# Kernel tuning notes

Measured on AMD Instinct MI355X. Metric: run time of the kernel, lower is better.

Reference implementation:

```python
import jax, jax.numpy as jnp
import numpy as np

B, T, C, H = 2, 2048, 1024, 16
D = C // H  # head dim = 64
NEG_MIN = jnp.finfo(jnp.float32).min


def setup_inputs() -> dict:
    key = jax.random.key(0)
    ks = jax.random.split(key, 5)
    std = 0.02
    return {
        "x": jax.random.normal(ks[0], (B, T, C), dtype=jnp.float32),
        "Wq": std * jax.random.normal(ks[1], (C, C), dtype=jnp.float32),
        "bq": jnp.zeros((C,), dtype=jnp.float32),
        "Wk": std * jax.random.normal(ks[2], (C, C), dtype=jnp.float32),
        "bk": jnp.zeros((C,), dtype=jnp.float32),
        "Wv": std * jax.random.normal(ks[3], (C, C), dtype=jnp.float32),
        "bv": jnp.zeros((C,), dtype=jnp.float32),
        "Wo": (std / np.sqrt(24.0)) * jax.random.normal(ks[4], (C, C), dtype=jnp.float32),
        "bo": jnp.zeros((C,), dtype=jnp.float32),
    }


def reference(x, Wq, bq, Wk, bk, Wv, bv, Wo, bo):
    # QKV projections -> (B, H, T, D)
    def proj(W, b):
        return (x @ W + b).reshape(B, T, H, D).transpose(0, 2, 1, 3)

    q = proj(Wq, bq)
    k = proj(Wk, bk)
    v = proj(Wv, bv)

    # full scores (B, H, T, T), causal mask, softmax
    attn = jnp.einsum("bhqd,bhkd->bhqk", q, k) / jnp.sqrt(jnp.float32(D))
    mask = jnp.tril(jnp.ones((T, T), dtype=bool))[None, None]
    attn = jnp.where(mask, attn, NEG_MIN)
    scores = jax.nn.softmax(attn, axis=-1)

    out = jnp.einsum("bhqk,bhkd->bhqd", scores, v)
    out = out.transpose(0, 2, 1, 3).reshape(B, T, C)
    return out @ Wo + bo
```

## Files before the change

### kernel.cpp

```cpp
#include <hip/hip_runtime.h>
#include <stdint.h>
#include <stddef.h>


#define B_SZ 2
#define T_SZ 2048
#define C_SZ 1024
#define H_SZ 16
#define D_SZ 64
#define M_SZ (B_SZ * T_SZ)
#define BHTD (B_SZ * H_SZ * T_SZ * D_SZ)
#define CC (C_SZ * C_SZ)

typedef __attribute__((ext_vector_type(8))) __bf16 bf16x8;
typedef __attribute__((ext_vector_type(4))) float f32x4;
typedef __attribute__((ext_vector_type(16))) float f32x16;

__device__ __forceinline__ unsigned short f2bf(float f) {
    union { float f; unsigned u; } v; v.f = f;
    v.u += 0x7fffu + ((v.u >> 16) & 1u);
    return (unsigned short)(v.u >> 16);
}

__device__ __forceinline__ unsigned pkbf(float lo, float hi_) {
    union { unsigned u; __bf16 h[2]; } r;
    r.h[0] = (__bf16)lo; r.h[1] = (__bf16)hi_;
    return r.u;
}

__device__ __forceinline__ float fexp2(float x) {
    float r;
    asm volatile("v_exp_f32 %0, %1\n\ts_nop 0" : "=v"(r) : "v"(x));
    return r;
}

__device__ __forceinline__ void load_lds16(const unsigned short* g, unsigned short* l) {
    __builtin_amdgcn_global_load_lds(
        (const __attribute__((address_space(1))) void*)g,
        (__attribute__((address_space(3))) void*)l, 16, 0, 0);
}


__global__ void cvt_x_kernel(const float4* __restrict__ in, ushort4* __restrict__ out, int n4) {
    int stride = gridDim.x * blockDim.x;
    for (int i = blockIdx.x * blockDim.x + threadIdx.x; i < n4; i += stride) {
        float4 v = in[i];
        ushort4 o;
        o.x = f2bf(v.x); o.y = f2bf(v.y); o.z = f2bf(v.z); o.w = f2bf(v.w);
        out[i] = o;
    }
}

__global__ __launch_bounds__(256) void transpose_cvt_kernel(
    const float* __restrict__ W0, const float* __restrict__ W1,
    const float* __restrict__ W2, const float* __restrict__ W3,
    unsigned short* __restrict__ T0, unsigned short* __restrict__ T1,
    unsigned short* __restrict__ T2, unsigned short* __restrict__ T3)
{
    __shared__ float tile[32][33];
    const float* W; unsigned short* Wt;
    switch (blockIdx.z) {
        case 0: W = W0; Wt = T0; break;
        case 1: W = W1; Wt = T1; break;
        case 2: W = W2; Wt = T2; break;
        default: W = W3; Wt = T3; break;
    }
    const int tx = threadIdx.x, ty = threadIdx.y;
    const int n0 = blockIdx.x * 32, k0 = blockIdx.y * 32;
    #pragma unroll
    for (int i = 0; i < 4; i++)
        tile[ty + i * 8][tx] = W[(size_t)(k0 + ty + i * 8) * C_SZ + n0 + tx];
    __syncthreads();
    #pragma unroll
    for (int i = 0; i < 4; i++)
        Wt[(size_t)(n0 + ty + i * 8) * C_SZ + k0 + tx] = f2bf(tile[tx][ty + i * 8]);
}

__global__ __launch_bounds__(256) void vt_kernel(
    const unsigned short* __restrict__ V, unsigned short* __restrict__ Vt)
{
    __shared__ unsigned short tile[32][33];
    const int bh = blockIdx.z;
    const int t0 = blockIdx.x * 32, d0 = blockIdx.y * 32;
    const unsigned short* src = V + (size_t)bh * T_SZ * D_SZ;
    unsigned short* dst = Vt + (size_t)bh * T_SZ * D_SZ;
    const int tx = threadIdx.x, ty = threadIdx.y;
    #pragma unroll
    for (int i = 0; i < 4; i++)
        tile[ty + i * 8][tx] = src[(size_t)(t0 + ty + i * 8) * D_SZ + d0 + tx];
    __syncthreads();
    #pragma unroll
    for (int i = 0; i < 4; i++)
        dst[(size_t)(d0 + ty + i * 8) * T_SZ + t0 + tx] = tile[tx][ty + i * 8];
}


__device__ __forceinline__ void gemm_tile_core(
    const unsigned short* __restrict__ A,
    const unsigned short* __restrict__ Bt,
    unsigned short* As, unsigned short* Bs,
    int m0, int n0, f32x4 acc[4][4])
{
    const int tid = threadIdx.x;
    const int lane = tid & 63;
    const int w = tid >> 6;
    const int l15 = lane & 15, lg = lane >> 4;
    const int wr = (w >> 1) * 64, wc = (w & 1) * 64;

    const unsigned short* Ag0 = A + (size_t)(m0 + (tid >> 2)) * C_SZ + (tid & 3) * 8;
    const unsigned short* Ag1 = Ag0 + (size_t)64 * C_SZ;
    const unsigned short* Bg0 = Bt + (size_t)(n0 + (tid >> 2)) * C_SZ + (tid & 3) * 8;
    const unsigned short* Bg1 = Bg0 + (size_t)64 * C_SZ;
    unsigned short* As0 = As + w * 512;
    unsigned short* As1 = As + 2048 + w * 512;
    unsigned short* Bs0 = Bs + w * 512;
    unsigned short* Bs1 = Bs + 2048 + w * 512;

    for (int k0 = 0; k0 < C_SZ; k0 += 32) {
        load_lds16(Ag0 + k0, As0);
        load_lds16(Ag1 + k0, As1);
        load_lds16(Bg0 + k0, Bs0);
        load_lds16(Bg1 + k0, Bs1);
        __syncthreads();
        bf16x8 af[4], bfv[4];
        const bf16x8* Ap = (const bf16x8*)As;
        const bf16x8* Bp = (const bf16x8*)Bs;
        #pragma unroll
        for (int m = 0; m < 4; m++) af[m] = Ap[(wr + m * 16 + l15) * 4 + lg];
        #pragma unroll
        for (int n = 0; n < 4; n++) bfv[n] = Bp[(wc + n * 16 + l15) * 4 + lg];
        #pragma unroll
        for (int m = 0; m < 4; m++)
            #pragma unroll
            for (int n = 0; n < 4; n++)
                acc[m][n] = __builtin_amdgcn_mfma_f32_16x16x32_bf16(af[m], bfv[n], acc[m][n], 0, 0, 0);
        __syncthreads();
    }
}

__global__ __launch_bounds__(256) void gemm_qkv_kernel(
    const unsigned short* __restrict__ A,
    const unsigned short* __restrict__ WtBase,
    const float* __restrict__ bq, const float* __restrict__ bk, const float* __restrict__ bv,
    unsigned short* __restrict__ QKV, unsigned short* __restrict__ Vtmp)
{
    __shared__ unsigned short As[4096], Bs[4096];
    const int z = blockIdx.x >> 3;
    const unsigned short* Bt = WtBase + (size_t)z * CC;
    const float* bias = (z == 0) ? bq : (z == 1) ? bk : bv;
    const float scale = (z == 0) ? 0.18033688011112042f : 1.0f;
    unsigned short* Out = (z == 2) ? Vtmp : QKV + (size_t)z * BHTD;

    f32x4 acc[4][4];
    f32x4 zero4 = {0.f, 0.f, 0.f, 0.f};
    #pragma unroll
    for (int m = 0; m < 4; m++)
        #pragma unroll
        for (int n = 0; n < 4; n++) acc[m][n] = zero4;

    const int m0 = blockIdx.y * 128, n0 = (blockIdx.x & 7) * 128;
    gemm_tile_core(A, Bt, As, Bs, m0, n0, acc);

    const int lane = threadIdx.x & 63;
    const int w = threadIdx.x >> 6;
    const int l15 = lane & 15, lg = lane >> 4;
    const int wr = (w >> 1) * 64, wc = (w & 1) * 64;
    #pragma unroll
    for (int n = 0; n < 4; n++) {
        const int col = n0 + wc + n * 16 + l15;
        const float bias_v = bias[col];
        const int h = col >> 6, d = col & 63;
        #pragma unroll
        for (int m = 0; m < 4; m++) {
            #pragma unroll
            for (int j = 0; j < 4; j++) {
                const int row = m0 + wr + m * 16 + lg * 4 + j;
                const int b = row >> 11, t = row & (T_SZ - 1);
                Out[(((size_t)(b * H_SZ + h)) * T_SZ + t) * D_SZ + d] =
                    f2bf((acc[m][n][j] + bias_v) * scale);
            }
        }
    }
}

__global__ __launch_bounds__(256) void gemm_out_kernel(
    const unsigned short* __restrict__ A,
    const unsigned short* __restrict__ Bt,
    const float* __restrict__ bo,
    float* __restrict__ Out)
{
    __shared__ unsigned short As[2048], Bs[4096];
    const int tid = threadIdx.x;
    const int lane = tid & 63;
    const int w = tid >> 6;
    const int l15 = lane & 15, lg = lane >> 4;
    const int wc = w * 32;
    const int m0 = blockIdx.y * 64, n0 = blockIdx.x * 128;

    const unsigned short* Ag  = A + (size_t)(m0 + (tid >> 2)) * C_SZ + (tid & 3) * 8;
    const unsigned short* Bg0 = Bt + (size_t)(n0 + (tid >> 2)) * C_SZ + (tid & 3) * 8;
    const unsigned short* Bg1 = Bg0 + (size_t)64 * C_SZ;
    unsigned short* As0 = As + w * 512;
    unsigned short* Bs0 = Bs + w * 512;
    unsigned short* Bs1 = Bs + 2048 + w * 512;

    f32x4 acc[4][2];
    f32x4 zero4 = {0.f, 0.f, 0.f, 0.f};
    #pragma unroll
    for (int m = 0; m < 4; m++)
        #pragma unroll
        for (int n = 0; n < 2; n++) acc[m][n] = zero4;

    for (int k0 = 0; k0 < C_SZ; k0 += 32) {
        load_lds16(Ag + k0, As0);
        load_lds16(Bg0 + k0, Bs0);
        load_lds16(Bg1 + k0, Bs1);
        __syncthreads();
        bf16x8 af[4], bfv[2];
        const bf16x8* Ap = (const bf16x8*)As;
        const bf16x8* Bp = (const bf16x8*)Bs;
        #pragma unroll
        for (int m = 0; m < 4; m++) af[m] = Ap[(m * 16 + l15) * 4 + lg];
        #pragma unroll
        for (int n = 0; n < 2; n++) bfv[n] = Bp[(wc + n * 16 + l15) * 4 + lg];
        #pragma unroll
        for (int m = 0; m < 4; m++)
            #pragma unroll
            for (int n = 0; n < 2; n++)
                acc[m][n] = __builtin_amdgcn_mfma_f32_16x16x32_bf16(af[m], bfv[n], acc[m][n], 0, 0, 0);
        __syncthreads();
    }

    #pragma unroll
    for (int n = 0; n < 2; n++) {
        const int col = n0 + wc + n * 16 + l15;
        const float bias_v = bo[col];
        #pragma unroll
        for (int m = 0; m < 4; m++) {
            #pragma unroll
            for (int j = 0; j < 4; j++) {
                const int row = m0 + m * 16 + lg * 4 + j;
                Out[(size_t)row * C_SZ + col] = acc[m][n][j] + bias_v;
            }
        }
    }
}

__global__ __launch_bounds__(256) void attn_fwd_kernel(
    const unsigned short* __restrict__ Q,
    const unsigned short* __restrict__ K,
    const unsigned short* __restrict__ Vt,
    unsigned short* __restrict__ O)
{
    const int idx = blockIdx.x;
    const int qt = (idx < 256) ? (15 - (idx >> 5)) : ((idx - 256) >> 5);
    const int bh = idx & 31;
    const int w = threadIdx.x >> 6;
    const int lane = threadIdx.x & 63;
    const int l31 = lane & 31, hi = lane >> 5;
    const int qw = qt * 128 + 32 * w;

    const unsigned short* Qh = Q + (size_t)bh * T_SZ * D_SZ;
    const unsigned short* Kh = K + (size_t)bh * T_SZ * D_SZ;
    const unsigned short* Vh = Vt + (size_t)bh * T_SZ * D_SZ;

    __shared__ __align__(16) unsigned short smem[24576];

    const int c0 = w * 64 + lane;
    const int row0 = c0 >> 3;
    const int sw0 = (c0 & 7) ^ (row0 & 7);
    const int koff0 = row0 * 64 + sw0 * 8;
    const int voff0 = row0 * T_SZ + sw0 * 8;
    const int ldsb0 = w * 512;

    bf16x8 qf[4];
    #pragma unroll
    for (int j = 0; j < 4; j++)
        qf[j] = *(const bf16x8*)&Qh[(size_t)(qw + l31) * D_SZ + j * 16 + 8 * hi];

    f32x16 acc[2];
    #pragma unroll
    for (int r = 0; r < 16; r++) { acc[0][r] = 0.f; acc[1][r] = 0.f; }
    float mrun = -3.0e38f, lrun = 0.f;

    const int tlast = (qw + 31) >> 6;
    const int ntb = 2 * qt + 2;
    const int qrow = qw + l31;
    const int swl = l31 & 7;

    {
        load_lds16(Kh + koff0, smem + ldsb0);
        load_lds16(Kh + koff0 + 2048, smem + 2048 + ldsb0);
        load_lds16(Vh + voff0, smem + 4096 + ldsb0);
        load_lds16(Vh + voff0 + 32 * T_SZ, smem + 6144 + ldsb0);
        const unsigned short* Kt = Kh + (size_t)64 * D_SZ;
        const unsigned short* Vtt = Vh + 64;
        load_lds16(Kt + koff0, smem + 8192 + ldsb0);
        load_lds16(Kt + koff0 + 2048, smem + 10240 + ldsb0);
        load_lds16(Vtt + voff0, smem + 12288 + ldsb0);
        load_lds16(Vtt + voff0 + 32 * T_SZ, smem + 14336 + ldsb0);
    }

    for (int tt = 0; tt < ntb; ++tt) {
        if (tt + 2 < ntb) {
            unsigned short* Bd = smem + ((tt + 2) % 3) * 8192;
            const unsigned short* Kt = Kh + (size_t)(tt + 2) * 64 * D_SZ;
            const unsigned short* Vtt = Vh + (tt + 2) * 64;
            load_lds16(Kt + koff0, Bd + ldsb0);
            load_lds16(Kt + koff0 + 2048, Bd + 2048 + ldsb0);
            load_lds16(Vtt + voff0, Bd + 4096 + ldsb0);
            load_lds16(Vtt + voff0 + 32 * T_SZ, Bd + 6144 + ldsb0);
            asm volatile("s_waitcnt vmcnt(8)" ::: "memory");
        } else if (tt + 1 < ntb) {
            asm volatile("s_waitcnt vmcnt(4)" ::: "memory");
        } else {
            asm volatile("s_waitcnt vmcnt(0)" ::: "memory");
        }
        __builtin_amdgcn_s_barrier();

        if (tt <= tlast) {
            const unsigned short* Ks = smem + (tt % 3) * 8192;
            const unsigned short* Vs = Ks + 4096;
            const int k0 = tt * 64;

            f32x16 s[2];
            #pragma unroll
            for (int kb = 0; kb < 2; ++kb) {
                bf16x8 kf[4];
                #pragma unroll
                for (int j = 0; j < 4; ++j) {
                    const int ch = (j * 2 + hi) ^ swl;
                    kf[j] = *(const bf16x8*)&Ks[(kb * 32 + l31) * 64 + ch * 8];
                }
                f32x16 sc;
                #pragma unroll
                for (int r = 0; r < 16; r++) sc[r] = 0.f;
                #pragma unroll
                for (int j = 0; j < 4; ++j)
                    sc = __builtin_amdgcn_mfma_f32_32x32x16_bf16(kf[j], qf[j], sc, 0, 0, 0);
                s[kb] = sc;
            }

            if (k0 + 63 > qw) {
                #pragma unroll
                for (int kb = 0; kb < 2; ++kb)
                    #pragma unroll
                    for (int r = 0; r < 16; ++r) {
                        const int kv = k0 + kb * 32 + (r & 3) + 8 * (r >> 2) + 4 * hi;
                        s[kb][r] = (kv > qrow) ? -3.0e38f : s[kb][r];
                    }
            }

            float pm0 = fmaxf(s[0][0], s[1][0]), pm1 = fmaxf(s[0][1], s[1][1]);
            float pm2 = fmaxf(s[0][2], s[1][2]), pm3 = fmaxf(s[0][3], s[1][3]);
            #pragma unroll
            for (int r = 4; r < 16; r += 4) {
                pm0 = fmaxf(pm0, fmaxf(s[0][r + 0], s[1][r + 0]));
                pm1 = fmaxf(pm1, fmaxf(s[0][r + 1], s[1][r + 1]));
                pm2 = fmaxf(pm2, fmaxf(s[0][r + 2], s[1][r + 2]));
                pm3 = fmaxf(pm3, fmaxf(s[0][r + 3], s[1][r + 3]));
            }
            float pm = fmaxf(fmaxf(pm0, pm1), fmaxf(pm2, pm3));
            pm = fmaxf(pm, __shfl_xor(pm, 32));

            if (!__all(pm <= mrun + 8.0f)) {
                const float mnew = fmaxf(mrun, pm);
                const float al = fexp2(mrun - mnew);
                lrun *= al;
                #pragma unroll
                for (int r = 0; r < 16; r++) { acc[0][r] *= al; acc[1][r] *= al; }
                mrun = mnew;
            }

            #pragma unroll
            for (int kb = 0; kb < 2; ++kb)
                #pragma unroll
                for (int r = 0; r < 16; r++) s[kb][r] = fexp2(s[kb][r] - mrun);
            float ps0 = s[0][0] + s[1][0], ps1 = s[0][1] + s[1][1];
            float ps2 = s[0][2] + s[1][2], ps3 = s[0][3] + s[1][3];
            #pragma unroll
            for (int r = 4; r < 16; r += 4) {
                ps0 += s[0][r + 0] + s[1][r + 0];
                ps1 += s[0][r + 1] + s[1][r + 1];
                ps2 += s[0][r + 2] + s[1][r + 2];
                ps3 += s[0][r + 3] + s[1][r + 3];
            }
            float ps = (ps0 + ps1) + (ps2 + ps3);
            ps += __shfl_xor(ps, 32);
            lrun += ps;

            bf16x8 pf[2][2];
            #pragma unroll
            for (int kb = 0; kb < 2; ++kb) {
                #pragma unroll
                for (int ksl = 0; ksl < 2; ++ksl) {
                    unsigned a0 = pkbf(s[kb][8 * ksl + 0], s[kb][8 * ksl + 1]);
                    unsigned a1 = pkbf(s[kb][8 * ksl + 2], s[kb][8 * ksl + 3]);
                    unsigned b0 = pkbf(s[kb][8 * ksl + 4], s[kb][8 * ksl + 5]);
                    unsigned b1 = pkbf(s[kb][8 * ksl + 6], s[kb][8 * ksl + 7]);
                    asm volatile("v_permlane32_swap_b32 %0, %1" : "+v"(a0), "+v"(b0));
                    asm volatile("v_permlane32_swap_b32 %0, %1" : "+v"(a1), "+v"(b1));
                    union { unsigned u[4]; bf16x8 v; } fr;
                    fr.u[0] = a0; fr.u[1] = a1; fr.u[2] = b0; fr.u[3] = b1;
                    pf[kb][ksl] = fr.v;
                }
            }

            #pragma unroll
            for (int dt = 0; dt < 2; ++dt)
                #pragma unroll
                for (int kb = 0; kb < 2; ++kb)
                    #pragma unroll
                    for (int ksl = 0; ksl < 2; ++ksl) {
                        const int ks = kb * 2 + ksl;
                        const int ch = (ks * 2 + hi) ^ swl;
                        const bf16x8 vf = *(const bf16x8*)&Vs[(dt * 32 + l31) * 64 + ch * 8];
                        acc[dt] = __builtin_amdgcn_mfma_f32_32x32x16_bf16(vf, pf[kb][ksl], acc[dt], 0, 0, 0);
                    }
        }
        __builtin_amdgcn_s_barrier();
    }

    unsigned short* ot = smem + w * 2304;
    const float inv = 1.0f / lrun;
    #pragma unroll
    for (int g = 0; g < 4; g++) {
        ushort4 wa, wb;
        wa.x = f2bf(acc[0][4 * g + 0] * inv); wa.y = f2bf(acc[0][4 * g + 1] * inv);
        wa.z = f2bf(acc[0][4 * g + 2] * inv); wa.w = f2bf(acc[0][4 * g + 3] * inv);
        wb.x = f2bf(acc[1][4 * g + 0] * inv); wb.y = f2bf(acc[1][4 * g + 1] * inv);
        wb.z = f2bf(acc[1][4 * g + 2] * inv); wb.w = f2bf(acc[1][4 * g + 3] * inv);
        *(ushort4*)&ot[l31 * 72 + 8 * g + 4 * hi] = wa;
        *(ushort4*)&ot[l31 * 72 + 32 + 8 * g + 4 * hi] = wb;
    }
    const int b = bh >> 4, h = bh & 15;
    #pragma unroll
    for (int pss = 0; pss < 4; pss++) {
        const int q = pss * 8 + (lane >> 3);
        const uint4 val = *(const uint4*)&ot[q * 72 + (lane & 7) * 8];
        *(uint4*)&O[((size_t)(b * T_SZ + qw + q)) * C_SZ + h * D_SZ + (lane & 7) * 8] = val;
    }
}


extern "C" void kernel_launch(void* const* d_in, const int* in_sizes, int n_in,
                              void* d_out, int out_size, void* d_ws, size_t ws_size,
                              hipStream_t stream)
{
    const float* x  = (const float*)d_in[0];
    const float* Wq = (const float*)d_in[1];
    const float* bq = (const float*)d_in[2];
    const float* Wk = (const float*)d_in[3];
    const float* bk = (const float*)d_in[4];
    const float* Wv = (const float*)d_in[5];
    const float* bv = (const float*)d_in[6];
    const float* Wo = (const float*)d_in[7];
    const float* bo = (const float*)d_in[8];

    uint8_t* ws = (uint8_t*)d_ws;
    unsigned short* XB   = (unsigned short*)(ws);
    unsigned short* WT   = (unsigned short*)(ws + (8u  << 20));
    unsigned short* QKV  = (unsigned short*)(ws + (16u << 20));
    unsigned short* Vtmp = (unsigned short*)(ws + (40u << 20));

    cvt_x_kernel<<<2048, 256, 0, stream>>>((const float4*)x, (ushort4*)XB, M_SZ * C_SZ / 4);
    transpose_cvt_kernel<<<dim3(32, 32, 4), dim3(32, 8), 0, stream>>>(
        Wq, Wk, Wv, Wo, WT, WT + CC, WT + 2 * (size_t)CC, WT + 3 * (size_t)CC);
    gemm_qkv_kernel<<<dim3(24, 32), 256, 0, stream>>>(XB, WT, bq, bk, bv, QKV, Vtmp);
    vt_kernel<<<dim3(64, 2, 32), dim3(32, 8), 0, stream>>>(Vtmp, QKV + 2 * (size_t)BHTD);
    attn_fwd_kernel<<<512, 256, 0, stream>>>(
        QKV, QKV + BHTD, QKV + 2 * (size_t)BHTD, Vtmp);
    gemm_out_kernel<<<dim3(8, 64), 256, 0, stream>>>(Vtmp, WT + 3 * (size_t)CC, bo, (float*)d_out);
}
```

Baseline: 121.4 us.

## Split causal attention KV range into two halves and merge partial outputs

The attention kernel now launches twice as many blocks. Each block handles half of the key/value tiles for its query tile and writes a bf16 partial output plus its running max and sum. A new merge kernel combines the two halves with softmax rescaling before the output projection. The K/V LDS buffering drops from three stages to two, and s_setprio is raised around the MFMA sections. The aim is better load balance and occupancy, at the cost of an extra kernel, extra global traffic for the partials (stored in d_out and XB scratch), and an added bf16 rounding step.

```diff
diff --git a/kernel.cpp b/kernel.cpp
--- a/kernel.cpp
+++ b/kernel.cpp
@@ -11,6 +11,7 @@
 #define M_SZ (B_SZ * T_SZ)
 #define BHTD (B_SZ * H_SZ * T_SZ * D_SZ)
 #define CC (C_SZ * C_SZ)
+#define MLQ 65536
 
 typedef __attribute__((ext_vector_type(8))) __bf16 bf16x8;
 typedef __attribute__((ext_vector_type(4))) float f32x4;
@@ -20,6 +21,11 @@
     union { float f; unsigned u; } v; v.f = f;
     v.u += 0x7fffu + ((v.u >> 16) & 1u);
     return (unsigned short)(v.u >> 16);
+}
+
+__device__ __forceinline__ float bf2f(unsigned short u) {
+    union { unsigned u; float f; } v; v.u = (unsigned)u << 16;
+    return v.f;
 }
 
 __device__ __forceinline__ unsigned pkbf(float lo, float hi_) {
@@ -250,11 +256,13 @@
     const unsigned short* __restrict__ Q,
     const unsigned short* __restrict__ K,
     const unsigned short* __restrict__ Vt,
-    unsigned short* __restrict__ O)
+    unsigned short* __restrict__ Opart,
+    float* __restrict__ Ml)
 {
     const int idx = blockIdx.x;
-    const int qt = (idx < 256) ? (15 - (idx >> 5)) : ((idx - 256) >> 5);
     const int bh = idx & 31;
+    const int qt = 15 - ((idx >> 5) & 15);
+    const int half = idx >> 9;
     const int w = threadIdx.x >> 6;
     const int lane = threadIdx.x & 63;
     const int l31 = lane & 31, hi = lane >> 5;
@@ -264,7 +272,7 @@
     const unsigned short* Kh = K + (size_t)bh * T_SZ * D_SZ;
     const unsigned short* Vh = Vt + (size_t)bh * T_SZ * D_SZ;
 
-    __shared__ __align__(16) unsigned short smem[24576];
+    __shared__ __align__(16) unsigned short smem[16384];
 
     const int c0 = w * 64 + lane;
     const int row0 = c0 >> 3;
@@ -284,34 +292,30 @@
     float mrun = -3.0e38f, lrun = 0.f;
 
     const int tlast = (qw + 31) >> 6;
-    const int ntb = 2 * qt + 2;
+    const int t0h = half * (qt + 1);
+    const int tend = t0h + qt + 1;
     const int qrow = qw + l31;
     const int swl = l31 & 7;
 
     {
-        load_lds16(Kh + koff0, smem + ldsb0);
-        load_lds16(Kh + koff0 + 2048, smem + 2048 + ldsb0);
-        load_lds16(Vh + voff0, smem + 4096 + ldsb0);
-        load_lds16(Vh + voff0 + 32 * T_SZ, smem + 6144 + ldsb0);
-        const unsigned short* Kt = Kh + (size_t)64 * D_SZ;
-        const unsigned short* Vtt = Vh + 64;
-        load_lds16(Kt + koff0, smem + 8192 + ldsb0);
-        load_lds16(Kt + koff0 + 2048, smem + 10240 + ldsb0);
-        load_lds16(Vtt + voff0, smem + 12288 + ldsb0);
-        load_lds16(Vtt + voff0 + 32 * T_SZ, smem + 14336 + ldsb0);
-    }
-
-    for (int tt = 0; tt < ntb; ++tt) {
-        if (tt + 2 < ntb) {
-            unsigned short* Bd = smem + ((tt + 2) % 3) * 8192;
-            const unsigned short* Kt = Kh + (size_t)(tt + 2) * 64 * D_SZ;
-            const unsigned short* Vtt = Vh + (tt + 2) * 64;
+        const unsigned short* Kt = Kh + (size_t)t0h * 64 * D_SZ;
+        const unsigned short* Vtt = Vh + t0h * 64;
+        unsigned short* Bd = smem + (t0h & 1) * 8192;
+        load_lds16(Kt + koff0, Bd + ldsb0);
+        load_lds16(Kt + koff0 + 2048, Bd + 2048 + ldsb0);
+        load_lds16(Vtt + voff0, Bd + 4096 + ldsb0);
+        load_lds16(Vtt + voff0 + 32 * T_SZ, Bd + 6144 + ldsb0);
+    }
+
+    for (int tt = t0h; tt < tend; ++tt) {
+        if (tt + 1 < tend) {
+            unsigned short* Bd = smem + ((tt + 1) & 1) * 8192;
+            const unsigned short* Kt = Kh + (size_t)(tt + 1) * 64 * D_SZ;
+            const unsigned short* Vtt = Vh + (tt + 1) * 64;
             load_lds16(Kt + koff0, Bd + ldsb0);
             load_lds16(Kt + koff0 + 2048, Bd + 2048 + ldsb0);
             load_lds16(Vtt + voff0, Bd + 4096 + ldsb0);
             load_lds16(Vtt + voff0 + 32 * T_SZ, Bd + 6144 + ldsb0);
-            asm volatile("s_waitcnt vmcnt(8)" ::: "memory");
-        } else if (tt + 1 < ntb) {
             asm volatile("s_waitcnt vmcnt(4)" ::: "memory");
         } else {
             asm volatile("s_waitcnt vmcnt(0)" ::: "memory");
@@ -319,11 +323,12 @@
         __builtin_amdgcn_s_barrier();
 
         if (tt <= tlast) {
-            const unsigned short* Ks = smem + (tt % 3) * 8192;
+            const unsigned short* Ks = smem + (tt & 1) * 8192;
             const unsigned short* Vs = Ks + 4096;
             const int k0 = tt * 64;
 
             f32x16 s[2];
+            __builtin_amdgcn_s_setprio(1);
             #pragma unroll
             for (int kb = 0; kb < 2; ++kb) {
                 bf16x8 kf[4];
@@ -340,6 +345,7 @@
                     sc = __builtin_amdgcn_mfma_f32_32x32x16_bf16(kf[j], qf[j], sc, 0, 0, 0);
                 s[kb] = sc;
             }
+            __builtin_amdgcn_s_setprio(0);
 
             if (k0 + 63 > qw) {
                 #pragma unroll
@@ -406,6 +412,7 @@
                 }
             }
 
+            __builtin_amdgcn_s_setprio(1);
             #pragma unroll
             for (int dt = 0; dt < 2; ++dt)
                 #pragma unroll
@@ -417,12 +424,13 @@
                         const bf16x8 vf = *(const bf16x8*)&Vs[(dt * 32 + l31) * 64 + ch * 8];
                         acc[dt] = __builtin_amdgcn_mfma_f32_32x32x16_bf16(vf, pf[kb][ksl], acc[dt], 0, 0, 0);
                     }
+            __builtin_amdgcn_s_setprio(0);
         }
         __builtin_amdgcn_s_barrier();
     }
 
     unsigned short* ot = smem + w * 2304;
-    const float inv = 1.0f / lrun;
+    const float inv = (lrun > 0.f) ? 1.0f / lrun : 0.f;
     #pragma unroll
     for (int g = 0; g < 4; g++) {
         ushort4 wa, wb;
@@ -433,13 +441,48 @@
         *(ushort4*)&ot[l31 * 72 + 8 * g + 4 * hi] = wa;
         *(ushort4*)&ot[l31 * 72 + 32 + 8 * g + 4 * hi] = wb;
     }
+    if (hi == 0) {
+        Ml[half * MLQ + bh * 2048 + qw + l31] = mrun;
+        Ml[2 * MLQ + half * MLQ + bh * 2048 + qw + l31] = lrun;
+    }
+    unsigned short* Op = Opart + (size_t)half * ((size_t)M_SZ * C_SZ);
     const int b = bh >> 4, h = bh & 15;
     #pragma unroll
     for (int pss = 0; pss < 4; pss++) {
         const int q = pss * 8 + (lane >> 3);
         const uint4 val = *(const uint4*)&ot[q * 72 + (lane & 7) * 8];
-        *(uint4*)&O[((size_t)(b * T_SZ + qw + q)) * C_SZ + h * D_SZ + (lane & 7) * 8] = val;
-    }
+        *(uint4*)&Op[((size_t)(b * T_SZ + qw + q)) * C_SZ + h * D_SZ + (lane & 7) * 8] = val;
+    }
+}
+
+__global__ __launch_bounds__(256) void merge_kernel(
+    const unsigned short* __restrict__ Opart,
+    const float* __restrict__ Ml,
+    unsigned short* __restrict__ Out)
+{
+    const int idx = blockIdx.x * 256 + threadIdx.x;
+    const int r = idx >> 7;
+    const int cc = (idx & 127) * 8;
+    const int b = r >> 11, t = r & (T_SZ - 1);
+    const int h = cc >> 6;
+    const int bh = b * H_SZ + h;
+    const float m0 = Ml[bh * 2048 + t];
+    const float m1 = Ml[MLQ + bh * 2048 + t];
+    const float l0 = Ml[2 * MLQ + bh * 2048 + t];
+    const float l1 = Ml[3 * MLQ + bh * 2048 + t];
+    const float M = fmaxf(m0, m1);
+    const float w0 = fexp2(m0 - M) * l0;
+    const float w1 = fexp2(m1 - M) * l1;
+    const float inv = 1.0f / (w0 + w1);
+    const float a0 = w0 * inv, a1 = w1 * inv;
+    const size_t off = (size_t)r * C_SZ + cc;
+    union { uint4 v; unsigned short u[8]; } p0, p1, o;
+    p0.v = *(const uint4*)&Opart[off];
+    p1.v = *(const uint4*)&Opart[(size_t)M_SZ * C_SZ + off];
+    #pragma unroll
+    for (int i = 0; i < 8; i++)
+        o.u[i] = f2bf(a0 * bf2f(p0.u[i]) + a1 * bf2f(p1.u[i]));
+    *(uint4*)&Out[off] = o.v;
 }
 
 
@@ -468,7 +511,10 @@
         Wq, Wk, Wv, Wo, WT, WT + CC, WT + 2 * (size_t)CC, WT + 3 * (size_t)CC);
     gemm_qkv_kernel<<<dim3(24, 32), 256, 0, stream>>>(XB, WT, bq, bk, bv, QKV, Vtmp);
     vt_kernel<<<dim3(64, 2, 32), dim3(32, 8), 0, stream>>>(Vtmp, QKV + 2 * (size_t)BHTD);
-    attn_fwd_kernel<<<512, 256, 0, stream>>>(
-        QKV, QKV + BHTD, QKV + 2 * (size_t)BHTD, Vtmp);
+    attn_fwd_kernel<<<1024, 256, 0, stream>>>(
+        QKV, QKV + BHTD, QKV + 2 * (size_t)BHTD,
+        (unsigned short*)d_out, (float*)XB);
+    merge_kernel<<<2048, 256, 0, stream>>>(
+        (const unsigned short*)d_out, (const float*)XB, Vtmp);
     gemm_out_kernel<<<dim3(8, 64), 256, 0, stream>>>(Vtmp, WT + 3 * (size_t)CC, bo, (float*)d_out);
 }
```

Result: no change. 122.2 us (+0.6%).

## Split attention KV range across two wave groups with in-block softmax merge

Applied to the files above, without the earlier changes.

Doubles the attention block to 512 threads. Two groups of four waves each process half of the KV tiles for the same 128-query tile, with double buffering per group instead of a shared triple buffer. Partial accumulators, maxima and sums are then merged through LDS using a log-sum-exp combine. MFMA sections are also wrapped in s_setprio raises. This gives each wave a shorter serial KV loop, at the cost of extra LDS, barriers and a merge epilogue, and it may lower occupancy.

```diff
diff --git a/kernel.cpp b/kernel.cpp
--- a/kernel.cpp
+++ b/kernel.cpp
@@ -246,7 +246,7 @@
     }
 }
 
-__global__ __launch_bounds__(256) void attn_fwd_kernel(
+__global__ __launch_bounds__(512) void attn_fwd_kernel(
     const unsigned short* __restrict__ Q,
     const unsigned short* __restrict__ K,
     const unsigned short* __restrict__ Vt,
@@ -255,23 +255,26 @@
     const int idx = blockIdx.x;
     const int qt = (idx < 256) ? (15 - (idx >> 5)) : ((idx - 256) >> 5);
     const int bh = idx & 31;
-    const int w = threadIdx.x >> 6;
+    const int w8 = threadIdx.x >> 6;
+    const int grp = w8 >> 2;
+    const int wg = w8 & 3;
     const int lane = threadIdx.x & 63;
     const int l31 = lane & 31, hi = lane >> 5;
-    const int qw = qt * 128 + 32 * w;
+    const int qw = qt * 128 + 32 * wg;
 
     const unsigned short* Qh = Q + (size_t)bh * T_SZ * D_SZ;
     const unsigned short* Kh = K + (size_t)bh * T_SZ * D_SZ;
     const unsigned short* Vh = Vt + (size_t)bh * T_SZ * D_SZ;
 
-    __shared__ __align__(16) unsigned short smem[24576];
-
-    const int c0 = w * 64 + lane;
+    __shared__ __align__(16) unsigned short smem[32768];
+
+    const int c0 = wg * 64 + lane;
     const int row0 = c0 >> 3;
     const int sw0 = (c0 & 7) ^ (row0 & 7);
     const int koff0 = row0 * 64 + sw0 * 8;
     const int voff0 = row0 * T_SZ + sw0 * 8;
-    const int ldsb0 = w * 512;
+    const int ldsb0 = wg * 512;
+    unsigned short* gbase = smem + grp * 16384;
 
     bf16x8 qf[4];
     #pragma unroll
@@ -284,46 +287,43 @@
     float mrun = -3.0e38f, lrun = 0.f;
 
     const int tlast = (qw + 31) >> 6;
-    const int ntb = 2 * qt + 2;
+    const int ntb = qt + 1;
+    const int tg0 = grp * ntb;
     const int qrow = qw + l31;
     const int swl = l31 & 7;
 
     {
-        load_lds16(Kh + koff0, smem + ldsb0);
-        load_lds16(Kh + koff0 + 2048, smem + 2048 + ldsb0);
-        load_lds16(Vh + voff0, smem + 4096 + ldsb0);
-        load_lds16(Vh + voff0 + 32 * T_SZ, smem + 6144 + ldsb0);
-        const unsigned short* Kt = Kh + (size_t)64 * D_SZ;
-        const unsigned short* Vtt = Vh + 64;
-        load_lds16(Kt + koff0, smem + 8192 + ldsb0);
-        load_lds16(Kt + koff0 + 2048, smem + 10240 + ldsb0);
-        load_lds16(Vtt + voff0, smem + 12288 + ldsb0);
-        load_lds16(Vtt + voff0 + 32 * T_SZ, smem + 14336 + ldsb0);
+        const unsigned short* Kt = Kh + (size_t)tg0 * 64 * D_SZ;
+        const unsigned short* Vtt = Vh + tg0 * 64;
+        load_lds16(Kt + koff0, gbase + ldsb0);
+        load_lds16(Kt + koff0 + 2048, gbase + 2048 + ldsb0);
+        load_lds16(Vtt + voff0, gbase + 4096 + ldsb0);
+        load_lds16(Vtt + voff0 + 32 * T_SZ, gbase + 6144 + ldsb0);
     }
 
     for (int tt = 0; tt < ntb; ++tt) {
-        if (tt + 2 < ntb) {
-            unsigned short* Bd = smem + ((tt + 2) % 3) * 8192;
-            const unsigned short* Kt = Kh + (size_t)(tt + 2) * 64 * D_SZ;
-            const unsigned short* Vtt = Vh + (tt + 2) * 64;
+        const int tg = tg0 + tt;
+        if (tt + 1 < ntb) {
+            unsigned short* Bd = gbase + ((tt + 1) & 1) * 8192;
+            const unsigned short* Kt = Kh + (size_t)(tg + 1) * 64 * D_SZ;
+            const unsigned short* Vtt = Vh + (tg + 1) * 64;
             load_lds16(Kt + koff0, Bd + ldsb0);
             load_lds16(Kt + koff0 + 2048, Bd + 2048 + ldsb0);
             load_lds16(Vtt + voff0, Bd + 4096 + ldsb0);
             load_lds16(Vtt + voff0 + 32 * T_SZ, Bd + 6144 + ldsb0);
-            asm volatile("s_waitcnt vmcnt(8)" ::: "memory");
-        } else if (tt + 1 < ntb) {
             asm volatile("s_waitcnt vmcnt(4)" ::: "memory");
         } else {
             asm volatile("s_waitcnt vmcnt(0)" ::: "memory");
         }
         __builtin_amdgcn_s_barrier();
 
-        if (tt <= tlast) {
-            const unsigned short* Ks = smem + (tt % 3) * 8192;
+        if (tg <= tlast) {
+            const unsigned short* Ks = gbase + (tt & 1) * 8192;
             const unsigned short* Vs = Ks + 4096;
-            const int k0 = tt * 64;
+            const int k0 = tg * 64;
 
             f32x16 s[2];
+            __builtin_amdgcn_s_setprio(1);
             #pragma unroll
             for (int kb = 0; kb < 2; ++kb) {
                 bf16x8 kf[4];
@@ -340,6 +340,7 @@
                     sc = __builtin_amdgcn_mfma_f32_32x32x16_bf16(kf[j], qf[j], sc, 0, 0, 0);
                 s[kb] = sc;
             }
+            __builtin_amdgcn_s_setprio(0);
 
             if (k0 + 63 > qw) {
                 #pragma unroll
@@ -406,6 +407,7 @@
                 }
             }
 
+            __builtin_amdgcn_s_setprio(1);
             #pragma unroll
             for (int dt = 0; dt < 2; ++dt)
                 #pragma unroll
@@ -417,28 +419,60 @@
                         const bf16x8 vf = *(const bf16x8*)&Vs[(dt * 32 + l31) * 64 + ch * 8];
                         acc[dt] = __builtin_amdgcn_mfma_f32_32x32x16_bf16(vf, pf[kb][ksl], acc[dt], 0, 0, 0);
                     }
+            __builtin_amdgcn_s_setprio(0);
         }
         __builtin_amdgcn_s_barrier();
     }
 
-    unsigned short* ot = smem + w * 2304;
-    const float inv = 1.0f / lrun;
-    #pragma unroll
-    for (int g = 0; g < 4; g++) {
-        ushort4 wa, wb;
-        wa.x = f2bf(acc[0][4 * g + 0] * inv); wa.y = f2bf(acc[0][4 * g + 1] * inv);
-        wa.z = f2bf(acc[0][4 * g + 2] * inv); wa.w = f2bf(acc[0][4 * g + 3] * inv);
-        wb.x = f2bf(acc[1][4 * g + 0] * inv); wb.y = f2bf(acc[1][4 * g + 1] * inv);
-        wb.z = f2bf(acc[1][4 * g + 2] * inv); wb.w = f2bf(acc[1][4 * g + 3] * inv);
-        *(ushort4*)&ot[l31 * 72 + 8 * g + 4 * hi] = wa;
-        *(ushort4*)&ot[l31 * 72 + 32 + 8 * g + 4 * hi] = wb;
-    }
-    const int b = bh >> 4, h = bh & 15;
-    #pragma unroll
-    for (int pss = 0; pss < 4; pss++) {
-        const int q = pss * 8 + (lane >> 3);
-        const uint4 val = *(const uint4*)&ot[q * 72 + (lane & 7) * 8];
-        *(uint4*)&O[((size_t)(b * T_SZ + qw + q)) * C_SZ + h * D_SZ + (lane & 7) * 8] = val;
+    float* accf = (float*)smem;
+    float* msh = accf + 256 * 33;
+    float* lsh = msh + 128;
+    if (grp == 1) {
+        const int li = wg * 64 + lane;
+        #pragma unroll
+        for (int r = 0; r < 16; r++) {
+            accf[li * 33 + r] = acc[0][r];
+            accf[li * 33 + 16 + r] = acc[1][r];
+        }
+        if (hi == 0) { msh[wg * 32 + l31] = mrun; lsh[wg * 32 + l31] = lrun; }
+    }
+    __builtin_amdgcn_s_barrier();
+    if (grp == 0) {
+        const int li = wg * 64 + lane;
+        const float m1 = msh[wg * 32 + l31];
+        const float l1 = lsh[wg * 32 + l31];
+        const float M = fmaxf(mrun, m1);
+        const float e0 = fexp2(mrun - M);
+        const float e1 = fexp2(m1 - M);
+        const float lm = e0 * lrun + e1 * l1;
+        const float inv = 1.0f / lm;
+        #pragma unroll
+        for (int r = 0; r < 16; r++) {
+            acc[0][r] = (e0 * acc[0][r] + e1 * accf[li * 33 + r]) * inv;
+            acc[1][r] = (e0 * acc[1][r] + e1 * accf[li * 33 + 16 + r]) * inv;
+        }
+    }
+    __builtin_amdgcn_s_barrier();
+
+    if (grp == 0) {
+        unsigned short* ot = smem + wg * 2304;
+        #pragma unroll
+        for (int g = 0; g < 4; g++) {
+            ushort4 wa, wb;
+            wa.x = f2bf(acc[0][4 * g + 0]); wa.y = f2bf(acc[0][4 * g + 1]);
+            wa.z = f2bf(acc[0][4 * g + 2]); wa.w = f2bf(acc[0][4 * g + 3]);
+            wb.x = f2bf(acc[1][4 * g + 0]); wb.y = f2bf(acc[1][4 * g + 1]);
+            wb.z = f2bf(acc[1][4 * g + 2]); wb.w = f2bf(acc[1][4 * g + 3]);
+            *(ushort4*)&ot[l31 * 72 + 8 * g + 4 * hi] = wa;
+            *(ushort4*)&ot[l31 * 72 + 32 + 8 * g + 4 * hi] = wb;
+        }
+        const int b = bh >> 4, h = bh & 15;
+        #pragma unroll
+        for (int pss = 0; pss < 4; pss++) {
+            const int q = pss * 8 + (lane >> 3);
+            const uint4 val = *(const uint4*)&ot[q * 72 + (lane & 7) * 8];
+            *(uint4*)&O[((size_t)(b * T_SZ + qw + q)) * C_SZ + h * D_SZ + (lane & 7) * 8] = val;
+        }
     }
 }
 
@@ -468,7 +502,7 @@
         Wq, Wk, Wv, Wo, WT, WT + CC, WT + 2 * (size_t)CC, WT + 3 * (size_t)CC);
     gemm_qkv_kernel<<<dim3(24, 32), 256, 0, stream>>>(XB, WT, bq, bk, bv, QKV, Vtmp);
     vt_kernel<<<dim3(64, 2, 32), dim3(32, 8), 0, stream>>>(Vtmp, QKV + 2 * (size_t)BHTD);
-    attn_fwd_kernel<<<512, 256, 0, stream>>>(
+    attn_fwd_kernel<<<512, 512, 0, stream>>>(
         QKV, QKV + BHTD, QKV + 2 * (size_t)BHTD, Vtmp);
     gemm_out_kernel<<<dim3(8, 64), 256, 0, stream>>>(Vtmp, WT + 3 * (size_t)CC, bo, (float*)d_out);
 }
```

Result: no change. 119.1 us (-1.9%).
